# Kernel tuning notes

Hardware: AMD Instinct MI355X
Metric: run time of the kernel (lower is better)

Reference implementation:

```python
import jax, jax.numpy as jnp
import numpy as np

N = 50000
E = 800000
NODE_IN = 64
EDGE_IN = 8
OUT = 1
SAGE_DIMS = [(64, 64), (64, 64), (64, 32), (32, 32)]
EDGE_DIMS = [(8, 64), (64, 64), (64, 32), (32, 32)]


def setup_inputs():
    key = jax.random.key(0)
    keys = iter(jax.random.split(key, 64))
    d = {}
    d["x"] = jax.random.normal(next(keys), (N, NODE_IN), jnp.float32)
    d["dis"] = jax.random.normal(next(keys), (E, EDGE_IN), jnp.float32)
    d["edge_index"] = jax.random.randint(next(keys), (2, E), 0, N, dtype=jnp.int32)
    for i, (fi, fo) in enumerate(SAGE_DIMS):
        d[f"s{i}_wl"] = jax.random.normal(next(keys), (fi, fo), jnp.float32) / np.sqrt(fi).astype(np.float32)
        d[f"s{i}_bl"] = jnp.zeros((fo,), jnp.float32)
        d[f"s{i}_wr"] = jax.random.normal(next(keys), (fi, fo), jnp.float32) / np.sqrt(fi).astype(np.float32)
    for i, (fi, h) in enumerate(EDGE_DIMS):
        d[f"e{i}_w1"] = jax.random.normal(next(keys), (fi, 2 * h), jnp.float32) / np.sqrt(fi).astype(np.float32)
        d[f"e{i}_b1"] = jnp.zeros((2 * h,), jnp.float32)
        d[f"e{i}_w2"] = jax.random.normal(next(keys), (2 * h, h), jnp.float32) / np.sqrt(2 * h).astype(np.float32)
        d[f"e{i}_b2"] = jnp.zeros((h,), jnp.float32)
    d["fc_w"] = jax.random.normal(next(keys), (64, OUT), jnp.float32) / 8.0
    d["fc_b"] = jnp.zeros((OUT,), jnp.float32)
    return d


def _sage(x, row, col, wl, bl, wr):
    # PyG SAGEConv (aggr='mean'): lin_l(mean_{j->i} x_j) + lin_r(x_i); lin_l has bias.
    msg = x[row]  # [E, F] gather of source features
    s = jax.ops.segment_sum(msg, col, num_segments=N)
    cnt = jax.ops.segment_sum(jnp.ones((row.shape[0], 1), x.dtype), col, num_segments=N)
    mean = s / jnp.maximum(cnt, 1.0)  # isolated nodes -> 0 (matches scatter-mean)
    return mean @ wl + bl + x @ wr


def _edge_conv(dis, col, w1, b1, w2, b2):
    # EdgeOnlyConv: add_self_loops with num_nodes=E and zero edge_attr, so the
    # output has E rows; self-loop message = lin(0) = b1 and each segment t gets
    # mean = (sum_{edges->t} lin(dis) + b1) / (deg_in(t) + 1); then lin_update.
    msg = dis @ w1 + b1  # [E, 2h]
    s = jax.ops.segment_sum(msg, col, num_segments=E)
    deg = jax.ops.segment_sum(jnp.ones((col.shape[0], 1), dis.dtype), col, num_segments=E)
    aggr = (s + b1) / (deg + 1.0)
    return aggr @ w2 + b2


def _forward(x, dis, edge_index, sage_params, edge_params, fc_w, fc_b):
    row, col = edge_index[0], edge_index[1]
    h = x
    for wl, bl, wr in sage_params:
        h = jax.nn.leaky_relu(_sage(h, row, col, wl, bl, wr))
    d = dis
    for w1, b1, w2, b2 in edge_params:
        d = jax.nn.leaky_relu(_edge_conv(d, col, w1, b1, w2, b2))
    # dropout is identity at inference
    feats = jnp.concatenate([h[row] * h[col], d], axis=1)  # [E, hidden]
    return feats @ fc_w + fc_b


def reference(x, dis, edge_index, s0_wl, s0_bl, s0_wr, s1_wl, s1_bl, s1_wr, s2_wl, s2_bl, s2_wr, s3_wl, s3_bl, s3_wr, e0_w1, e0_b1, e0_w2, e0_b2, e1_w1, e1_b1, e1_w2, e1_b2, e2_w1, e2_b1, e2_w2, e2_b2, e3_w1, e3_b1, e3_w2, e3_b2, fc_w, fc_b):
    sage_params = [(s0_wl, s0_bl, s0_wr), (s1_wl, s1_bl, s1_wr), (s2_wl, s2_bl, s2_wr), (s3_wl, s3_bl, s3_wr)]
    edge_params = [(e0_w1, e0_b1, e0_w2, e0_b2), (e1_w1, e1_b1, e1_w2, e1_b2), (e2_w1, e2_b1, e2_w2, e2_b2), (e3_w1, e3_b1, e3_w2, e3_b2)]
    return _forward(x, dis, edge_index, sage_params, edge_params, fc_w, fc_b)
```

## Files before the change

### kernel.cpp

```cpp
#include <hip/hip_runtime.h>

#define LRELU(v) ((v) > 0.0f ? (v) : 0.01f * (v))


__global__ void bucket_count_k(const int* __restrict__ col, int* __restrict__ bcnt, int E) {
    __shared__ int lcnt[512];
    int tid = threadIdx.x;
    for (int i = tid; i < 512; i += 1024) lcnt[i] = 0;
    __syncthreads();
    int base = blockIdx.x * 8192;
    for (int k = 0; k < 8; ++k) {
        int e = base + k * 1024 + tid;
        if (e < E) atomicAdd(&lcnt[col[e] >> 7], 1);
    }
    __syncthreads();
    for (int i = tid; i < 512; i += 1024) {
        int v = lcnt[i];
        if (v) atomicAdd(&bcnt[i], v);
    }
}

__global__ void bucket_scan_k(const int* __restrict__ bcnt, int* __restrict__ bbase,
                              int* __restrict__ bwp, int NBUCK, int E) {
    __shared__ int s[512];
    int tid = threadIdx.x;
    int v = (tid < NBUCK) ? bcnt[tid] : 0;
    s[tid] = v;
    __syncthreads();
    for (int off = 1; off < 512; off <<= 1) {
        int t = (tid >= off) ? s[tid - off] : 0;
        __syncthreads();
        s[tid] += t;
        __syncthreads();
    }
    if (tid < NBUCK) {
        int ex = s[tid] - v;
        bbase[tid] = ex;
        bwp[tid] = ex;
    }
    if (tid == 0) bbase[NBUCK] = E;
}

__global__ void bucket_scatter_k(const int* __restrict__ row, const int* __restrict__ col,
                                 int* __restrict__ bwp, int2* __restrict__ tmp, int E) {
    __shared__ int lcnt[512];
    __shared__ int gbase[512];
    int tid = threadIdx.x;
    for (int i = tid; i < 512; i += 1024) lcnt[i] = 0;
    __syncthreads();
    int base = blockIdx.x * 8192;
    int lpos[8], bk[8];
    for (int k = 0; k < 8; ++k) {
        int e = base + k * 1024 + tid;
        if (e < E) {
            int b = col[e] >> 7;
            bk[k] = b;
            lpos[k] = atomicAdd(&lcnt[b], 1);
        } else
            bk[k] = -1;
    }
    __syncthreads();
    for (int i = tid; i < 512; i += 1024) {
        int v = lcnt[i];
        gbase[i] = v ? atomicAdd(&bwp[i], v) : 0;
    }
    __syncthreads();
    for (int k = 0; k < 8; ++k) {
        int e = base + k * 1024 + tid;
        if (e < E) {
            int c = col[e];
            tmp[gbase[bk[k]] + lpos[k]] = make_int2(row[e], ((c & 127) << 25) | e);
        }
    }
}

__global__ void bucket_csr_k(const int2* __restrict__ tmp, const int* __restrict__ bbase,
                             int* __restrict__ rowptr, int* __restrict__ cnt,
                             int2* __restrict__ pairs, int N, int E) {
    constexpr int CAP = 6144;
    __shared__ int2 buf[CAP];
    __shared__ int lcnt[128];
    __shared__ int sscan[128];
    __shared__ int lwp[128];
    int b = blockIdx.x;
    int tid = threadIdx.x;
    int s = bbase[b], e = bbase[b + 1];
    int sz = e - s;
    if (tid < 128) lcnt[tid] = 0;
    __syncthreads();
    for (int i = tid; i < sz; i += 256) {
        int2 v = tmp[s + i];
        if (i < CAP) buf[i] = v;
        atomicAdd(&lcnt[((unsigned)v.y) >> 25], 1);
    }
    __syncthreads();
    if (tid < 128) sscan[tid] = lcnt[tid];
    __syncthreads();
    for (int off = 1; off < 128; off <<= 1) {
        int t = (tid < 128 && tid >= off) ? sscan[tid - off] : 0;
        __syncthreads();
        if (tid < 128) sscan[tid] += t;
        __syncthreads();
    }
    if (tid < 128) {
        int ex = sscan[tid] - lcnt[tid];
        lwp[tid] = ex;
        int c = b * 128 + tid;
        if (c < N) {
            rowptr[c] = s + ex;
            cnt[c] = lcnt[tid];
            if (c == N - 1) rowptr[N] = E;
        }
    }
    __syncthreads();
    for (int i = tid; i < sz; i += 256) {
        int2 v = (i < CAP) ? buf[i] : tmp[s + i];
        int cl = ((unsigned)v.y) >> 25;
        int p = atomicAdd(&lwp[cl], 1);
        pairs[s + p] = make_int2(v.x, v.y & 0x1FFFFFF);
    }
}

template <int FIN, int FOUT>
__global__ void gemm2_k(const float* __restrict__ h, const float* __restrict__ wl,
                        const float* __restrict__ wr, const float* __restrict__ bl,
                        float* __restrict__ hl, float* __restrict__ hr, int N) {
    constexpr int XT = (2 * FOUT) / 4;
    constexpr int YT = 256 / XT;
    constexpr int NPT = 4;
    constexpr int NPB = YT * NPT;
    __shared__ float sw[FIN * 2 * FOUT];
    int lin = threadIdx.y * XT + threadIdx.x;
    for (int idx = lin; idx < FIN * FOUT; idx += 256) {
        int f = idx / FOUT, o = idx % FOUT;
        sw[f * 2 * FOUT + o] = wl[idx];
        sw[f * 2 * FOUT + FOUT + o] = wr[idx];
    }
    __syncthreads();
    int og = threadIdx.x * 4;
    int base = blockIdx.x * NPB + threadIdx.y * NPT;
    int ix[NPT] = {min(base + 0, N - 1), min(base + 1, N - 1), min(base + 2, N - 1),
                   min(base + 3, N - 1)};
    float4 s[NPT] = {{0.f, 0.f, 0.f, 0.f}, {0.f, 0.f, 0.f, 0.f}, {0.f, 0.f, 0.f, 0.f},
                     {0.f, 0.f, 0.f, 0.f}};
#pragma unroll 2
    for (int f = 0; f < FIN; f += 4) {
        float4 w0 = *(const float4*)&sw[(f + 0) * 2 * FOUT + og];
        float4 w1 = *(const float4*)&sw[(f + 1) * 2 * FOUT + og];
        float4 w2 = *(const float4*)&sw[(f + 2) * 2 * FOUT + og];
        float4 w3 = *(const float4*)&sw[(f + 3) * 2 * FOUT + og];
#pragma unroll
        for (int k = 0; k < NPT; ++k) {
            float4 v = *(const float4*)(h + (size_t)ix[k] * FIN + f);
            s[k].x += v.x * w0.x + v.y * w1.x + v.z * w2.x + v.w * w3.x;
            s[k].y += v.x * w0.y + v.y * w1.y + v.z * w2.y + v.w * w3.y;
            s[k].z += v.x * w0.z + v.y * w1.z + v.z * w2.z + v.w * w3.z;
            s[k].w += v.x * w0.w + v.y * w1.w + v.z * w2.w + v.w * w3.w;
        }
    }
    bool isR = og >= FOUT;
    int oo = isR ? og - FOUT : og;
    float4 bias = {0.f, 0.f, 0.f, 0.f};
    if (isR) bias = *(const float4*)&bl[oo];
    float* dst = isR ? hr : hl;
#pragma unroll
    for (int k = 0; k < NPT; ++k) {
        int i = base + k;
        if (i < N) {
            float4 r = {s[k].x + bias.x, s[k].y + bias.y, s[k].z + bias.z, s[k].w + bias.w};
            *(float4*)(dst + (size_t)i * FOUT + oo) = r;
        }
    }
}

__global__ void aggr_fused64_k(const float* __restrict__ hl, const float* __restrict__ hr,
                               const int* __restrict__ rowptr, const int2* __restrict__ pairs,
                               float* __restrict__ out, int N) {
    int wave = (blockIdx.x * blockDim.x + threadIdx.x) >> 6;
    int lane = threadIdx.x & 63;
    if (wave >= N) return;
    int u = lane >> 4, f4 = lane & 15;
    int s = rowptr[wave], e = rowptr[wave + 1];
    float4 a = {0.f, 0.f, 0.f, 0.f};
    for (int p = s + u; p < e; p += 4) {
        const float4* hp = (const float4*)(hl + (size_t)pairs[p].x * 64);
        float4 v = hp[f4];
        a.x += v.x; a.y += v.y; a.z += v.z; a.w += v.w;
    }
    a.x += __shfl_down(a.x, 32); a.y += __shfl_down(a.y, 32);
    a.z += __shfl_down(a.z, 32); a.w += __shfl_down(a.w, 32);
    a.x += __shfl_down(a.x, 16); a.y += __shfl_down(a.y, 16);
    a.z += __shfl_down(a.z, 16); a.w += __shfl_down(a.w, 16);
    if (lane < 16) {
        float inv = 1.0f / fmaxf((float)(e - s), 1.0f);
        float4 r = ((const float4*)(hr + (size_t)wave * 64))[f4];
        float4 o;
        o.x = LRELU(a.x * inv + r.x);
        o.y = LRELU(a.y * inv + r.y);
        o.z = LRELU(a.z * inv + r.z);
        o.w = LRELU(a.w * inv + r.w);
        ((float4*)(out + (size_t)wave * 64))[f4] = o;
    }
}

__global__ void aggr_fused32_k(const float* __restrict__ hl, const float* __restrict__ hr,
                               const int* __restrict__ rowptr, const int2* __restrict__ pairs,
                               float* __restrict__ out, int N) {
    int wave = (blockIdx.x * blockDim.x + threadIdx.x) >> 6;
    int lane = threadIdx.x & 63;
    if (wave >= N) return;
    int u = lane >> 3, f4 = lane & 7;
    int s = rowptr[wave], e = rowptr[wave + 1];
    float4 a = {0.f, 0.f, 0.f, 0.f};
    for (int p = s + u; p < e; p += 8) {
        const float4* hp = (const float4*)(hl + (size_t)pairs[p].x * 32);
        float4 v = hp[f4];
        a.x += v.x; a.y += v.y; a.z += v.z; a.w += v.w;
    }
    a.x += __shfl_down(a.x, 32); a.y += __shfl_down(a.y, 32);
    a.z += __shfl_down(a.z, 32); a.w += __shfl_down(a.w, 32);
    a.x += __shfl_down(a.x, 16); a.y += __shfl_down(a.y, 16);
    a.z += __shfl_down(a.z, 16); a.w += __shfl_down(a.w, 16);
    a.x += __shfl_down(a.x, 8); a.y += __shfl_down(a.y, 8);
    a.z += __shfl_down(a.z, 8); a.w += __shfl_down(a.w, 8);
    if (lane < 8) {
        float inv = 1.0f / fmaxf((float)(e - s), 1.0f);
        float4 r = ((const float4*)(hr + (size_t)wave * 32))[f4];
        float4 o;
        o.x = LRELU(a.x * inv + r.x);
        o.y = LRELU(a.y * inv + r.y);
        o.z = LRELU(a.z * inv + r.z);
        o.w = LRELU(a.w * inv + r.w);
        ((float4*)(out + (size_t)wave * 32))[f4] = o;
    }
}

__global__ void edge_aggr8_k(const float* __restrict__ dis, const int* __restrict__ rowptr,
                             const int2* __restrict__ pairs, float* __restrict__ sd, int N) {
    int wave = (blockIdx.x * blockDim.x + threadIdx.x) >> 6;
    int lane = threadIdx.x & 63;
    if (wave >= N) return;
    int u = lane >> 1, f4 = lane & 1;
    int s = rowptr[wave], e = rowptr[wave + 1];
    float4 a = {0.f, 0.f, 0.f, 0.f};
    for (int p = s + u; p < e; p += 32) {
        const float4* dp = (const float4*)(dis + (size_t)pairs[p].y * 8);
        float4 v = dp[f4];
        a.x += v.x; a.y += v.y; a.z += v.z; a.w += v.w;
    }
    for (int off = 32; off >= 2; off >>= 1) {
        a.x += __shfl_down(a.x, off); a.y += __shfl_down(a.y, off);
        a.z += __shfl_down(a.z, off); a.w += __shfl_down(a.w, off);
    }
    if (lane < 2) ((float4*)(sd + (size_t)wave * 8))[f4] = a;
}

template <int H2, int HOUT>
__device__ __forceinline__ void w12_body(const float* __restrict__ w1,
                                         const float* __restrict__ w2, float* __restrict__ out,
                                         int i, int o) {
    float s = 0.0f;
#pragma unroll
    for (int k = 0; k < H2; ++k) s += w1[i * H2 + k] * w2[k * HOUT + o];
    out[i * HOUT + o] = s;
}

__global__ void gemm_w12_all_k(const float* __restrict__ w1_0, const float* __restrict__ w2_0,
                               float* __restrict__ o0, const float* __restrict__ w1_1,
                               const float* __restrict__ w2_1, float* __restrict__ o1,
                               const float* __restrict__ w1_2, const float* __restrict__ w2_2,
                               float* __restrict__ o2, const float* __restrict__ w1_3,
                               const float* __restrict__ w2_3, float* __restrict__ o3) {
    int b = blockIdx.x;
    int o = threadIdx.x;
    if (b < 8) {
        w12_body<128, 64>(w1_0, w2_0, o0, b, o);
    } else if (b < 72) {
        w12_body<128, 64>(w1_1, w2_1, o1, b - 8, o);
    } else if (b < 136) {
        if (o < 32) w12_body<64, 32>(w1_2, w2_2, o2, b - 72, o);
    } else {
        if (o < 32) w12_body<64, 32>(w1_3, w2_3, o3, b - 136, o);
    }
}

template <int FIN, int FOUT>
__global__ void edge_compute_scatter_k(const float* __restrict__ sd, const int* __restrict__ cnt,
                                       const float* __restrict__ w12, const float* __restrict__ mw2,
                                       const float* __restrict__ b1w2, const float* __restrict__ b2,
                                       const float* __restrict__ cnext,
                                       const int* __restrict__ col, float* __restrict__ sdnext,
                                       int N) {
    constexpr int ROWS = 256 / FOUT;
    constexpr int NPT = 4;
    constexpr int NPB = ROWS * NPT;
    __shared__ float sw[FIN * FOUT];
    int lin = threadIdx.y * FOUT + threadIdx.x;
    for (int idx = lin; idx < FIN * FOUT; idx += 256) sw[idx] = w12[idx];
    __syncthreads();
    int o = threadIdx.x;
    int base = blockIdx.x * NPB + threadIdx.y * NPT;
    int ix[NPT] = {min(base + 0, N - 1), min(base + 1, N - 1), min(base + 2, N - 1),
                   min(base + 3, N - 1)};
    float s[NPT] = {0.f, 0.f, 0.f, 0.f};
#pragma unroll 2
    for (int f = 0; f < FIN; f += 4) {
        float w0 = sw[(f + 0) * FOUT + o], w1 = sw[(f + 1) * FOUT + o];
        float w2 = sw[(f + 2) * FOUT + o], w3 = sw[(f + 3) * FOUT + o];
#pragma unroll
        for (int k = 0; k < NPT; ++k) {
            float4 v = *(const float4*)(sd + (size_t)ix[k] * FIN + f);
            s[k] += v.x * w0 + v.y * w1 + v.z * w2 + v.w * w3;
        }
    }
    float mo = mw2[o], bo = b1w2[o], b2o = b2[o], co = cnext[o];
#pragma unroll
    for (int k = 0; k < NPT; ++k) {
        int i = base + k;
        if (i < N) {
            float deg = (float)cnt[i];
            float inv = 1.0f / (deg + 1.0f);
            float val = LRELU((s[k] + deg * mo + bo) * inv + b2o);
            atomicAdd(&sdnext[(size_t)col[i] * FOUT + o], val - co);
        }
    }
}

template <int FIN, int FOUT>
__global__ void edge_compute2_k(const float* __restrict__ sd, const int* __restrict__ cnt,
                                const float* __restrict__ w12, const float* __restrict__ mw2,
                                const float* __restrict__ b1w2, const float* __restrict__ b2,
                                float* __restrict__ out, int N) {
    constexpr int ROWS = 256 / FOUT;
    constexpr int NPT = 4;
    constexpr int NPB = ROWS * NPT;
    __shared__ float sw[FIN * FOUT];
    int lin = threadIdx.y * FOUT + threadIdx.x;
    for (int idx = lin; idx < FIN * FOUT; idx += 256) sw[idx] = w12[idx];
    __syncthreads();
    int o = threadIdx.x;
    int base = blockIdx.x * NPB + threadIdx.y * NPT;
    int ix[NPT] = {min(base + 0, N - 1), min(base + 1, N - 1), min(base + 2, N - 1),
                   min(base + 3, N - 1)};
    float s[NPT] = {0.f, 0.f, 0.f, 0.f};
#pragma unroll 2
    for (int f = 0; f < FIN; f += 4) {
        float w0 = sw[(f + 0) * FOUT + o], w1 = sw[(f + 1) * FOUT + o];
        float w2 = sw[(f + 2) * FOUT + o], w3 = sw[(f + 3) * FOUT + o];
#pragma unroll
        for (int k = 0; k < NPT; ++k) {
            float4 v = *(const float4*)(sd + (size_t)ix[k] * FIN + f);
            s[k] += v.x * w0 + v.y * w1 + v.z * w2 + v.w * w3;
        }
    }
    float mo = mw2[o], bo = b1w2[o], b2o = b2[o];
#pragma unroll
    for (int k = 0; k < NPT; ++k) {
        int i = base + k;
        if (i < N) {
            float deg = (float)cnt[i];
            float inv = 1.0f / (deg + 1.0f);
            out[(size_t)i * FOUT + o] = LRELU((s[k] + deg * mo + bo) * inv + b2o);
        }
    }
}

__global__ void consts_k(const float* __restrict__ e0_b1, const float* __restrict__ e0_w2,
                         const float* __restrict__ e0_b2, const float* __restrict__ e1_b1,
                         const float* __restrict__ e1_w2, const float* __restrict__ e1_b2,
                         const float* __restrict__ e2_b1, const float* __restrict__ e2_w2,
                         const float* __restrict__ e2_b2, const float* __restrict__ e3_b1,
                         const float* __restrict__ e3_w2, const float* __restrict__ e3_b2,
                         const float* __restrict__ w12_1, const float* __restrict__ w12_2,
                         const float* __restrict__ w12_3, float* __restrict__ cbuf) {
    __shared__ float c1[64], c2[64], c3[32];
    int tid = threadIdx.x;
    if (tid < 64) {
        float s = 0.0f;
#pragma unroll
        for (int k = 0; k < 128; ++k) s += e0_b1[k] * e0_w2[k * 64 + tid];
        cbuf[192 + tid] = s;
        c1[tid] = LRELU(s + e0_b2[tid]);
        cbuf[tid] = c1[tid];
    }
    if (tid < 64) {
        float s = 0.0f;
#pragma unroll
        for (int k = 0; k < 128; ++k) s += e1_b1[k] * e1_w2[k * 64 + tid];
        cbuf[256 + tid] = s;
        c2[tid] = LRELU(s + e1_b2[tid]);
        cbuf[64 + tid] = c2[tid];
    }
    if (tid < 32) {
        float s = 0.0f;
#pragma unroll
        for (int k = 0; k < 64; ++k) s += e2_b1[k] * e2_w2[k * 32 + tid];
        cbuf[384 + tid] = s;
        c3[tid] = LRELU(s + e2_b2[tid]);
        cbuf[128 + tid] = c3[tid];
    }
    if (tid < 32) {
        float s = 0.0f;
#pragma unroll
        for (int k = 0; k < 64; ++k) s += e3_b1[k] * e3_w2[k * 32 + tid];
        cbuf[448 + tid] = s;
        cbuf[160 + tid] = LRELU(s + e3_b2[tid]);
    }
    __syncthreads();
    if (tid < 64) {
        float s = cbuf[256 + tid];
#pragma unroll
        for (int f = 0; f < 64; ++f) s += c1[f] * w12_1[f * 64 + tid];
        cbuf[320 + tid] = s;
    }
    if (tid < 32) {
        float s = cbuf[384 + tid];
#pragma unroll
        for (int f = 0; f < 64; ++f) s += c2[f] * w12_2[f * 32 + tid];
        cbuf[416 + tid] = s;
    }
    if (tid < 32) {
        float s = cbuf[448 + tid];
#pragma unroll
        for (int f = 0; f < 32; ++f) s += c3[f] * w12_3[f * 32 + tid];
        cbuf[480 + tid] = s;
    }
}

__global__ void final_k(const float* __restrict__ h3, const float* __restrict__ dv3,
                        const float* __restrict__ c4, const int* __restrict__ row,
                        const int* __restrict__ col, const float* __restrict__ fcw,
                        const float* __restrict__ fcb, float* __restrict__ out, int E, int N) {
    __shared__ float sw[64];
    __shared__ float sc4[32];
    int tid = threadIdx.x;
    if (tid < 64) sw[tid] = fcw[tid];
    if (tid < 32) sc4[tid] = c4[tid];
    __syncthreads();
    int e = blockIdx.x * blockDim.x + tid;
    if (e >= E) return;
    int r = row[e], c = col[e];
    const float4* hr = (const float4*)(h3 + (size_t)r * 32);
    const float4* hc = (const float4*)(h3 + (size_t)c * 32);
    float s = fcb[0];
#pragma unroll
    for (int q = 0; q < 8; ++q) {
        float4 a = hr[q], b = hc[q];
        s += a.x * b.x * sw[q * 4 + 0] + a.y * b.y * sw[q * 4 + 1] + a.z * b.z * sw[q * 4 + 2] +
             a.w * b.w * sw[q * 4 + 3];
    }
    if (e < N) {
        const float4* dp = (const float4*)(dv3 + (size_t)e * 32);
#pragma unroll
        for (int q = 0; q < 8; ++q) {
            float4 d = dp[q];
            s += d.x * sw[32 + q * 4 + 0] + d.y * sw[32 + q * 4 + 1] + d.z * sw[32 + q * 4 + 2] +
                 d.w * sw[32 + q * 4 + 3];
        }
    } else {
#pragma unroll
        for (int k = 0; k < 32; ++k) s += sc4[k] * sw[32 + k];
    }
    out[e] = s;
}

extern "C" void kernel_launch(void* const* d_in, const int* in_sizes, int n_in, void* d_out,
                              int out_size, void* d_ws, size_t ws_size, hipStream_t stream) {
    const float* x = (const float*)d_in[0];
    const float* dis = (const float*)d_in[1];
    const int* ei = (const int*)d_in[2];
    const float* s_wl[4] = {(const float*)d_in[3], (const float*)d_in[6], (const float*)d_in[9],
                            (const float*)d_in[12]};
    const float* s_bl[4] = {(const float*)d_in[4], (const float*)d_in[7], (const float*)d_in[10],
                            (const float*)d_in[13]};
    const float* s_wr[4] = {(const float*)d_in[5], (const float*)d_in[8], (const float*)d_in[11],
                            (const float*)d_in[14]};
    const float* e_w1[4] = {(const float*)d_in[15], (const float*)d_in[19], (const float*)d_in[23],
                            (const float*)d_in[27]};
    const float* e_b1[4] = {(const float*)d_in[16], (const float*)d_in[20], (const float*)d_in[24],
                            (const float*)d_in[28]};
    const float* e_w2[4] = {(const float*)d_in[17], (const float*)d_in[21], (const float*)d_in[25],
                            (const float*)d_in[29]};
    const float* e_b2[4] = {(const float*)d_in[18], (const float*)d_in[22], (const float*)d_in[26],
                            (const float*)d_in[30]};
    const float* fcw = (const float*)d_in[31];
    const float* fcb = (const float*)d_in[32];

    const int N = in_sizes[0] / 64;
    const int E = in_sizes[1] / 8;
    const int* row = ei;
    const int* col = ei + E;
    const int NBUCK = (N + 127) / 128;
    const int EB = (E + 8191) / 8192;

    auto au = [](size_t v) { return (v + 255) & ~(size_t)255; };
    char* p = (char*)d_ws;
    int* cnt = (int*)p;       p += au((size_t)N * 4);
    int* rowptr = (int*)p;    p += au((size_t)(N + 1) * 4);
    int* bcnt = (int*)p;      p += au(512 * 4);
    int* bbase = (int*)p;     p += au(513 * 4);
    int* bwp = (int*)p;       p += au(512 * 4);
    float* w12_0 = (float*)p; p += au(512 * 4);
    float* w12_1 = (float*)p; p += au(4096 * 4);
    float* w12_2 = (float*)p; p += au(2048 * 4);
    float* w12_3 = (float*)p; p += au(1024 * 4);
    float* cbuf = (float*)p;  p += au(512 * 4);
    int2* pairs = (int2*)p;   p += au((size_t)E * 8);
    float* acc = (float*)p;   p += au((size_t)N * 64 * 4);
    float* hA = (float*)p;    p += au((size_t)N * 64 * 4);
    float* hB = (float*)p;    p += au((size_t)N * 64 * 4);
    float* dvA = (float*)p;   p += au((size_t)N * 64 * 4);
    float* dvB = (float*)p;   p += au((size_t)N * 64 * 4);

    int2* tmp = (int2*)dvA;

    hipMemsetAsync(bcnt, 0, 512 * 4, stream);
    bucket_count_k<<<EB, 1024, 0, stream>>>(col, bcnt, E);
    bucket_scan_k<<<1, 512, 0, stream>>>(bcnt, bbase, bwp, NBUCK, E);
    bucket_scatter_k<<<EB, 1024, 0, stream>>>(row, col, bwp, tmp, E);
    bucket_csr_k<<<NBUCK, 256, 0, stream>>>(tmp, bbase, rowptr, cnt, pairs, N, E);

    gemm_w12_all_k<<<168, 64, 0, stream>>>(e_w1[0], e_w2[0], w12_0, e_w1[1], e_w2[1], w12_1,
                                           e_w1[2], e_w2[2], w12_2, e_w1[3], e_w2[3], w12_3);
    consts_k<<<1, 128, 0, stream>>>(e_b1[0], e_w2[0], e_b2[0], e_b1[1], e_w2[1], e_b2[1], e_b1[2],
                                    e_w2[2], e_b2[2], e_b1[3], e_w2[3], e_b2[3], w12_1, w12_2,
                                    w12_3, cbuf);

    const int WPB = 4;

    gemm2_k<64, 64><<<(N + 31) / 32, dim3(32, 8), 0, stream>>>(x, s_wl[0], s_wr[0], s_bl[0], acc,
                                                               dvB, N);
    aggr_fused64_k<<<(N + WPB - 1) / WPB, 256, 0, stream>>>(acc, dvB, rowptr, pairs, hA, N);
    gemm2_k<64, 64><<<(N + 31) / 32, dim3(32, 8), 0, stream>>>(hA, s_wl[1], s_wr[1], s_bl[1], acc,
                                                               dvB, N);
    aggr_fused64_k<<<(N + WPB - 1) / WPB, 256, 0, stream>>>(acc, dvB, rowptr, pairs, hB, N);
    gemm2_k<64, 32><<<(N + 63) / 64, dim3(16, 16), 0, stream>>>(hB, s_wl[2], s_wr[2], s_bl[2], acc,
                                                                dvB, N);
    aggr_fused32_k<<<(N + WPB - 1) / WPB, 256, 0, stream>>>(acc, dvB, rowptr, pairs, hA, N);
    gemm2_k<32, 32><<<(N + 63) / 64, dim3(16, 16), 0, stream>>>(hA, s_wl[3], s_wr[3], s_bl[3], acc,
                                                                dvB, N);
    aggr_fused32_k<<<(N + WPB - 1) / WPB, 256, 0, stream>>>(acc, dvB, rowptr, pairs, hB, N);

    edge_aggr8_k<<<(N + WPB - 1) / WPB, 256, 0, stream>>>(dis, rowptr, pairs, acc, N);
    hipMemsetAsync(dvA, 0, (size_t)N * 64 * 4, stream);
    edge_compute_scatter_k<8, 64><<<(N + 15) / 16, dim3(64, 4), 0, stream>>>(
        acc, cnt, w12_0, cbuf + 192, cbuf + 192, e_b2[0], cbuf + 0, col, dvA, N);
    hipMemsetAsync(acc, 0, (size_t)N * 64 * 4, stream);
    edge_compute_scatter_k<64, 64><<<(N + 15) / 16, dim3(64, 4), 0, stream>>>(
        dvA, cnt, w12_1, cbuf + 320, cbuf + 256, e_b2[1], cbuf + 64, col, acc, N);
    hipMemsetAsync(dvA, 0, (size_t)N * 32 * 4, stream);
    edge_compute_scatter_k<64, 32><<<(N + 31) / 32, dim3(32, 8), 0, stream>>>(
        acc, cnt, w12_2, cbuf + 416, cbuf + 384, e_b2[2], cbuf + 128, col, dvA, N);
    edge_compute2_k<32, 32><<<(N + 31) / 32, dim3(32, 8), 0, stream>>>(
        dvA, cnt, w12_3, cbuf + 480, cbuf + 448, e_b2[3], dvB, N);

    final_k<<<(E + 255) / 256, 256, 0, stream>>>(hB, dvB, cbuf + 160, row, col, fcw, fcb,
                                                 (float*)d_out, E, N);
}
```

Measured before the change: 517.1 us.

## Store final node features in bf16 and process two edges per thread in final kernel

Adds a conversion kernel that rounds the last SAGE layer output to bf16 into a spare buffer. The final edge kernel then gathers half-size rows for both endpoints and handles two edges per thread, issuing loads early for more memory-level parallelism. It also precomputes the constant self-loop dot product once per block. This is meant to cut gather bandwidth in the final kernel, at the cost of an extra small kernel and reduced precision in the h[row]*h[col] term.

Result: faster. 505.6 us (-2.2%).

```diff
diff --git a/kernel.cpp b/kernel.cpp
--- a/kernel.cpp
+++ b/kernel.cpp
@@ -1,7 +1,6 @@
 #include <hip/hip_runtime.h>
 
 #define LRELU(v) ((v) > 0.0f ? (v) : 0.01f * (v))
-
 
 __global__ void bucket_count_k(const int* __restrict__ col, int* __restrict__ bcnt, int E) {
     __shared__ int lcnt[512];
@@ -427,41 +426,111 @@
     }
 }
 
-__global__ void final_k(const float* __restrict__ h3, const float* __restrict__ dv3,
+__global__ void tobf16_k(const float* __restrict__ src, unsigned short* __restrict__ dst, int n) {
+    int base = (blockIdx.x * 256 + threadIdx.x) * 4;
+    if (base >= n) return;
+    float4 v = *(const float4*)(src + base);
+    union { float f; unsigned u; } c;
+    unsigned short o[4];
+    c.f = v.x; o[0] = (unsigned short)((c.u + 0x7fffu + ((c.u >> 16) & 1)) >> 16);
+    c.f = v.y; o[1] = (unsigned short)((c.u + 0x7fffu + ((c.u >> 16) & 1)) >> 16);
+    c.f = v.z; o[2] = (unsigned short)((c.u + 0x7fffu + ((c.u >> 16) & 1)) >> 16);
+    c.f = v.w; o[3] = (unsigned short)((c.u + 0x7fffu + ((c.u >> 16) & 1)) >> 16);
+    *(ushort4*)(dst + base) = make_ushort4(o[0], o[1], o[2], o[3]);
+}
+
+__device__ __forceinline__ float b2f_lo(unsigned u) {
+    union { unsigned i; float f; } v;
+    v.i = u << 16;
+    return v.f;
+}
+__device__ __forceinline__ float b2f_hi(unsigned u) {
+    union { unsigned i; float f; } v;
+    v.i = u & 0xffff0000u;
+    return v.f;
+}
+__device__ __forceinline__ float bdot8(uint4 a, uint4 b, const float* __restrict__ w) {
+    return b2f_lo(a.x) * b2f_lo(b.x) * w[0] + b2f_hi(a.x) * b2f_hi(b.x) * w[1] +
+           b2f_lo(a.y) * b2f_lo(b.y) * w[2] + b2f_hi(a.y) * b2f_hi(b.y) * w[3] +
+           b2f_lo(a.z) * b2f_lo(b.z) * w[4] + b2f_hi(a.z) * b2f_hi(b.z) * w[5] +
+           b2f_lo(a.w) * b2f_lo(b.w) * w[6] + b2f_hi(a.w) * b2f_hi(b.w) * w[7];
+}
+
+__global__ void final_k(const unsigned short* __restrict__ h3b, const float* __restrict__ dv3,
                         const float* __restrict__ c4, const int* __restrict__ row,
                         const int* __restrict__ col, const float* __restrict__ fcw,
                         const float* __restrict__ fcb, float* __restrict__ out, int E, int N) {
     __shared__ float sw[64];
     __shared__ float sc4[32];
+    __shared__ float cdot_s;
     int tid = threadIdx.x;
     if (tid < 64) sw[tid] = fcw[tid];
     if (tid < 32) sc4[tid] = c4[tid];
     __syncthreads();
-    int e = blockIdx.x * blockDim.x + tid;
-    if (e >= E) return;
-    int r = row[e], c = col[e];
-    const float4* hr = (const float4*)(h3 + (size_t)r * 32);
-    const float4* hc = (const float4*)(h3 + (size_t)c * 32);
-    float s = fcb[0];
-#pragma unroll
-    for (int q = 0; q < 8; ++q) {
-        float4 a = hr[q], b = hc[q];
-        s += a.x * b.x * sw[q * 4 + 0] + a.y * b.y * sw[q * 4 + 1] + a.z * b.z * sw[q * 4 + 2] +
-             a.w * b.w * sw[q * 4 + 3];
-    }
-    if (e < N) {
-        const float4* dp = (const float4*)(dv3 + (size_t)e * 32);
-#pragma unroll
-        for (int q = 0; q < 8; ++q) {
-            float4 d = dp[q];
-            s += d.x * sw[32 + q * 4 + 0] + d.y * sw[32 + q * 4 + 1] + d.z * sw[32 + q * 4 + 2] +
-                 d.w * sw[32 + q * 4 + 3];
-        }
-    } else {
-#pragma unroll
-        for (int k = 0; k < 32; ++k) s += sc4[k] * sw[32 + k];
-    }
-    out[e] = s;
+    if (tid == 0) {
+        float cd = 0.0f;
+#pragma unroll
+        for (int k = 0; k < 32; ++k) cd += sc4[k] * sw[32 + k];
+        cdot_s = cd;
+    }
+    __syncthreads();
+    float fb = fcb[0];
+    float cdot = cdot_s;
+    int e0 = blockIdx.x * 512 + tid;
+    int e1 = e0 + 256;
+    bool v0 = e0 < E, v1 = e1 < E;
+    int r0 = 0, c0 = 0, r1 = 0, c1 = 0;
+    if (v0) { r0 = row[e0]; c0 = col[e0]; }
+    if (v1) { r1 = row[e1]; c1 = col[e1]; }
+    uint4 a00, a01, b00, b01, a10, a11, b10, b11;
+    if (v0) {
+        const uint4* pr = (const uint4*)(h3b + (size_t)r0 * 32);
+        const uint4* pc = (const uint4*)(h3b + (size_t)c0 * 32);
+        a00 = pr[0]; a01 = pr[1]; b00 = pc[0]; b01 = pc[1];
+    }
+    if (v1) {
+        const uint4* pr = (const uint4*)(h3b + (size_t)r1 * 32);
+        const uint4* pc = (const uint4*)(h3b + (size_t)c1 * 32);
+        a10 = pr[0]; a11 = pr[1]; b10 = pc[0]; b11 = pc[1];
+    }
+    if (v0) {
+        float s = fb + bdot8(a00, b00, sw) + bdot8(a01, b01, sw + 8) ;
+        const uint4* pr = (const uint4*)(h3b + (size_t)r0 * 32);
+        const uint4* pc = (const uint4*)(h3b + (size_t)c0 * 32);
+        uint4 a2 = pr[2], a3 = pr[3], b2 = pc[2], b3 = pc[3];
+        s += bdot8(a2, b2, sw + 16) + bdot8(a3, b3, sw + 24);
+        if (e0 < N) {
+            const float4* dp = (const float4*)(dv3 + (size_t)e0 * 32);
+#pragma unroll
+            for (int q = 0; q < 8; ++q) {
+                float4 d = dp[q];
+                s += d.x * sw[32 + q * 4 + 0] + d.y * sw[32 + q * 4 + 1] +
+                     d.z * sw[32 + q * 4 + 2] + d.w * sw[32 + q * 4 + 3];
+            }
+        } else {
+            s += cdot;
+        }
+        out[e0] = s;
+    }
+    if (v1) {
+        float s = fb + bdot8(a10, b10, sw) + bdot8(a11, b11, sw + 8);
+        const uint4* pr = (const uint4*)(h3b + (size_t)r1 * 32);
+        const uint4* pc = (const uint4*)(h3b + (size_t)c1 * 32);
+        uint4 a2 = pr[2], a3 = pr[3], b2 = pc[2], b3 = pc[3];
+        s += bdot8(a2, b2, sw + 16) + bdot8(a3, b3, sw + 24);
+        if (e1 < N) {
+            const float4* dp = (const float4*)(dv3 + (size_t)e1 * 32);
+#pragma unroll
+            for (int q = 0; q < 8; ++q) {
+                float4 d = dp[q];
+                s += d.x * sw[32 + q * 4 + 0] + d.y * sw[32 + q * 4 + 1] +
+                     d.z * sw[32 + q * 4 + 2] + d.w * sw[32 + q * 4 + 3];
+            }
+        } else {
+            s += cdot;
+        }
+        out[e1] = s;
+    }
 }
 
 extern "C" void kernel_launch(void* const* d_in, const int* in_sizes, int n_in, void* d_out,
@@ -513,6 +582,7 @@
     float* dvB = (float*)p;   p += au((size_t)N * 64 * 4);
 
     int2* tmp = (int2*)dvA;
+    unsigned short* h3b = (unsigned short*)hA;
 
     hipMemsetAsync(bcnt, 0, 512 * 4, stream);
     bucket_count_k<<<EB, 1024, 0, stream>>>(col, bcnt, E);
@@ -541,6 +611,8 @@
                                                                 dvB, N);
     aggr_fused32_k<<<(N + WPB - 1) / WPB, 256, 0, stream>>>(acc, dvB, rowptr, pairs, hB, N);
 
+    tobf16_k<<<(N * 32 / 4 + 255) / 256, 256, 0, stream>>>(hB, h3b, N * 32);
+
     edge_aggr8_k<<<(N + WPB - 1) / WPB, 256, 0, stream>>>(dis, rowptr, pairs, acc, N);
     hipMemsetAsync(dvA, 0, (size_t)N * 64 * 4, stream);
     edge_compute_scatter_k<8, 64><<<(N + 15) / 16, dim3(64, 4), 0, stream>>>(
@@ -554,6 +626,6 @@
     edge_compute2_k<32, 32><<<(N + 31) / 32, dim3(32, 8), 0, stream>>>(
         dvA, cnt, w12_3, cbuf + 480, cbuf + 448, e_b2[3], dvB, N);
 
-    final_k<<<(E + 255) / 256, 256, 0, stream>>>(hB, dvB, cbuf + 160, row, col, fcw, fcb,
+    final_k<<<(E + 511) / 512, 256, 0, stream>>>(h3b, dvB, cbuf + 160, row, col, fcw, fcb,
                                                  (float*)d_out, E, N);
 }
```
